# Performance work log

Hardware: AMD Instinct MI355X
Metric: run time of the kernel (lower is better)

Reference implementation:

```python
import jax, jax.numpy as jnp
import numpy as np

D_MODEL = 4096
D_FF = 14336
T = 8192


def setup_inputs() -> dict:
    key = jax.random.key(0)
    k1, k2, k3, k4, k5 = jax.random.split(key, 5)
    s_in = 1.0 / np.sqrt(D_MODEL)
    s_ff = 1.0 / np.sqrt(D_FF)
    return {
        "hidden_states": jax.random.normal(k1, (T, D_MODEL), dtype=jnp.float32),
        "routing_weights": jax.random.uniform(k2, (T, 1), dtype=jnp.float32),
        "w_gate": jax.random.normal(k3, (D_MODEL, D_FF), dtype=jnp.float32) * s_in,
        "w_up": jax.random.normal(k4, (D_MODEL, D_FF), dtype=jnp.float32) * s_in,
        "w_down": jax.random.normal(k5, (D_FF, D_MODEL), dtype=jnp.float32) * s_ff,
    }


def reference(hidden_states, routing_weights, w_gate, w_up, w_down):
    # SwiGLU expert MLP: down(silu(gate(x)) * up(x)), scaled by routing weight
    gate = jnp.einsum("td,df->tf", hidden_states, w_gate)  # [T, D_FF]
    up = jnp.einsum("td,df->tf", hidden_states, w_up)      # [T, D_FF]
    h = jax.nn.silu(gate) * up                               # fused SwiGLU
    out = jnp.einsum("tf,fd->td", h, w_down)                 # [T, D_MODEL]
    return routing_weights * out
```

## Files before the change

### kernel.cpp

```cpp
#include <hip/hip_runtime.h>
#include <hip/hip_bf16.h>

using bf16 = __hip_bfloat16;
typedef __attribute__((ext_vector_type(8))) short bf16x8;
typedef __attribute__((ext_vector_type(4))) float f32x4;
typedef __attribute__((ext_vector_type(4))) int i32x4;

#define T_DIM 8192
#define DM    4096
#define DFF   14336

#define MFMA(va, vb, vc) __builtin_amdgcn_mfma_f32_16x16x32_bf16(va, vb, vc, 0, 0, 0)

__device__ __forceinline__ void gld_lds16(const bf16* gsrc, bf16* ldst) {
  auto* g = (const __attribute__((address_space(1))) unsigned int*)gsrc;
  auto* l = (__attribute__((address_space(3))) unsigned int*)ldst;
  __builtin_amdgcn_global_load_lds(g, l, 16, 0, 0);
}

__device__ __forceinline__ void stage8k(const bf16* __restrict__ gbase, long lda,
                                        long grow0, long k0, bf16* lds_tile,
                                        int gran0, int tid) {
  const int g = gran0 + tid;
  const int row = g >> 3, c16 = g & 7;
  const bf16* src = gbase + (grow0 + row) * lda + k0 + ((long)(c16 ^ (row & 7)) << 3);
  bf16* dst = lds_tile + ((size_t)(gran0 + (tid & ~63)) << 3);
  gld_lds16(src, dst);
}

#define LDA8(PB, H, M, KK) (*(const bf16x8*)(aP##KK + (PB) + (H) * 16384 + (M) * 4096))
#define LDB8(PB, N, KK)    (*(const bf16x8*)(bP##KK + (PB) + (N) * 8192))

#define PHASE_MFMA_BEGIN()                            \
  __builtin_amdgcn_s_barrier();                       \
  asm volatile("s_waitcnt lgkmcnt(0)" ::: "memory");  \
  __builtin_amdgcn_sched_barrier(0);                  \
  __builtin_amdgcn_s_setprio(1)

#define PHASE_MFMA_END()                              \
  __builtin_amdgcn_s_setprio(0);                      \
  __builtin_amdgcn_sched_barrier(0);                  \
  __builtin_amdgcn_s_barrier()

__global__ void cast_pad_kernel(const float* __restrict__ in,
                                bf16* __restrict__ out, long xlda, int n8) {
  int idx = blockIdx.x * blockDim.x + threadIdx.x;
  int stride = gridDim.x * blockDim.x;
  for (int i = idx; i < n8; i += stride) {
    const int row = i >> 9;
    const int c8 = i & 511;
    const float4 v0 = reinterpret_cast<const float4*>(in)[(long)i * 2];
    const float4 v1 = reinterpret_cast<const float4*>(in)[(long)i * 2 + 1];
    bf16 t[8] = {__float2bfloat16(v0.x), __float2bfloat16(v0.y),
                 __float2bfloat16(v0.z), __float2bfloat16(v0.w),
                 __float2bfloat16(v1.x), __float2bfloat16(v1.y),
                 __float2bfloat16(v1.z), __float2bfloat16(v1.w)};
    *reinterpret_cast<bf16x8*>(&out[(long)row * xlda + (long)c8 * 8]) =
        *reinterpret_cast<bf16x8*>(t);
  }
}

__global__ void transpose_cast_kernel(const float* __restrict__ in,
                                      bf16* __restrict__ out, int R, int C,
                                      long out_lda) {
  __shared__ float tile[32][33];
  const int c0 = blockIdx.x * 32, r0 = blockIdx.y * 32;
  const int tx = threadIdx.x, ty = threadIdx.y;
#pragma unroll
  for (int j = 0; j < 4; ++j)
    tile[ty + j * 8][tx] = in[(long)(r0 + ty + j * 8) * C + (c0 + tx)];
  __syncthreads();
#pragma unroll
  for (int j = 0; j < 4; ++j)
    out[(long)(c0 + ty + j * 8) * out_lda + (r0 + tx)] =
        __float2bfloat16(tile[tx][ty + j * 8]);
}

__global__ __launch_bounds__(512, 2) void gemm_gateup_kernel(
    const bf16* __restrict__ X, const bf16* __restrict__ Gt,
    const bf16* __restrict__ Ut, bf16* __restrict__ H,
    long ldx, long ldw, long ldh) {
  __shared__ __align__(16) bf16 smem[4 * 256 * 64];

  const int tid = threadIdx.x;
  const int lane = tid & 63, wid = tid >> 6;
  const int wm = wid >> 2, wn = wid & 3;
  const int fr = lane & 15, fg = lane >> 4;

  const int id = blockIdx.x;
  const int fsub = id & 7, bm = id >> 3;
  const long row0 = (long)bm * 256;
  const int NK = DM / 64;

  bf16* const sAb = smem;
  bf16* const sBb = smem + 32768;

  const int inner0 = ((fg ^ (fr & 7)) << 4);
  const int inner1 = (((4 | fg) ^ (fr & 7)) << 4);
  const char* aP0 = (const char*)sAb + ((wm * 16 + fr) << 7) + inner0;
  const char* aP1 = (const char*)sAb + ((wm * 16 + fr) << 7) + inner1;
  const char* bP0 = (const char*)sBb + ((wn * 16 + fr) << 7) + inner0;
  const char* bP1 = (const char*)sBb + ((wn * 16 + fr) << 7) + inner1;

  const int r6 = tid >> 3;
  const long sc = (long)((tid & 7) ^ (r6 & 7)) << 3;
  const int tu = tid & ~63;
  const bf16* pS0 = X + (row0 + 128 + r6) * ldx + 64 + sc;
  const bf16* pS1 = X + (row0 + 192 + r6) * ldx + 64 + sc;
  const bf16* pS2 = X + (row0 +       r6) * ldx + 128 + sc;
  const bf16* pS3 = X + (row0 +  64 + r6) * ldx + 128 + sc;
  long fcol0 = (long)fsub * 128;
  const bf16* pS4 = Gt + (fcol0 +      r6) * ldw + 128 + sc;
  const bf16* pS5 = Gt + (fcol0 + 64 + r6) * ldw + 128 + sc;
  const bf16* pS6 = Ut + (fcol0 +      r6) * ldw + 128 + sc;
  const bf16* pS7 = Ut + (fcol0 + 64 + r6) * ldw + 128 + sc;

  for (int fb = 0; fb < 14; ++fb) {
    __builtin_amdgcn_s_barrier();

    f32x4 acc[8][4];
    const f32x4 z = {0.f, 0.f, 0.f, 0.f};
#pragma unroll
    for (int m = 0; m < 8; ++m)
#pragma unroll
      for (int n = 0; n < 4; ++n) acc[m][n] = z;

    stage8k(X, ldx, row0, 0, sAb, 0, tid);
    stage8k(X, ldx, row0, 0, sAb, 512, tid);
    stage8k(X, ldx, row0, 0, sAb, 1024, tid);
    stage8k(X, ldx, row0, 0, sAb, 1536, tid);
    stage8k(Gt, ldw, fcol0, 0, sBb, 0, tid);
    stage8k(Gt, ldw, fcol0, 0, sBb, 512, tid);
    stage8k(Ut, ldw, fcol0 - 128, 0, sBb, 1024, tid);
    stage8k(Ut, ldw, fcol0 - 128, 0, sBb, 1536, tid);
    stage8k(X, ldx, row0, 64, sAb + 16384, 0, tid);
    stage8k(X, ldx, row0, 64, sAb + 16384, 512, tid);
    stage8k(Gt, ldw, fcol0, 64, sBb + 16384, 0, tid);
    stage8k(Gt, ldw, fcol0, 64, sBb + 16384, 512, tid);
    stage8k(Ut, ldw, fcol0 - 128, 64, sBb + 16384, 1024, tid);
    stage8k(Ut, ldw, fcol0 - 128, 64, sBb + 16384, 1536, tid);
    asm volatile("s_waitcnt vmcnt(6)" ::: "memory");
    __builtin_amdgcn_s_barrier();

    bf16x8 a[4][2], b[4][2];
    int k1 = 64, k2 = 128;

#pragma unroll 2
    for (int t = 0; t < NK; ++t) {
      const int par = t & 1;
      const int pb = par << 15;
      bf16* aCur = sAb + par * 16384;
      bf16* bCur = sBb + par * 16384;
      bf16* aNxt = sAb + (par ^ 1) * 16384;

#pragma unroll
      for (int m = 0; m < 4; ++m) { a[m][0] = LDA8(pb, 0, m, 0); a[m][1] = LDA8(pb, 0, m, 1); }
#pragma unroll
      for (int n = 0; n < 2; ++n) { b[n][0] = LDB8(pb, n, 0); b[n][1] = LDB8(pb, n, 1); }
      gld_lds16(pS0, aNxt + ((1024 + tu) << 3));
      gld_lds16(pS1, aNxt + ((1536 + tu) << 3));
      PHASE_MFMA_BEGIN();
#pragma unroll
      for (int m = 0; m < 4; ++m)
#pragma unroll
        for (int n = 0; n < 2; ++n)
#pragma unroll
          for (int kk = 0; kk < 2; ++kk)
            acc[m][n] = MFMA(a[m][kk], b[n][kk], acc[m][n]);
      PHASE_MFMA_END();

#pragma unroll
      for (int n = 2; n < 4; ++n) { b[n][0] = LDB8(pb, n, 0); b[n][1] = LDB8(pb, n, 1); }
      gld_lds16(pS2, aCur + ((0 + tu) << 3));
      gld_lds16(pS3, aCur + ((512 + tu) << 3));
      PHASE_MFMA_BEGIN();
#pragma unroll
      for (int m = 0; m < 4; ++m)
#pragma unroll
        for (int n = 2; n < 4; ++n)
#pragma unroll
          for (int kk = 0; kk < 2; ++kk)
            acc[m][n] = MFMA(a[m][kk], b[n][kk], acc[m][n]);
      PHASE_MFMA_END();

#pragma unroll
      for (int m = 0; m < 4; ++m) { a[m][0] = LDA8(pb, 1, m, 0); a[m][1] = LDA8(pb, 1, m, 1); }
      gld_lds16(pS4, bCur + ((0 + tu) << 3));
      gld_lds16(pS5, bCur + ((512 + tu) << 3));
      PHASE_MFMA_BEGIN();
#pragma unroll
      for (int m = 0; m < 4; ++m)
#pragma unroll
        for (int n = 2; n < 4; ++n)
#pragma unroll
          for (int kk = 0; kk < 2; ++kk)
            acc[4 + m][n] = MFMA(a[m][kk], b[n][kk], acc[4 + m][n]);
      PHASE_MFMA_END();

      gld_lds16(pS6, bCur + ((1024 + tu) << 3));
      gld_lds16(pS7, bCur + ((1536 + tu) << 3));
      asm volatile("s_waitcnt vmcnt(6)" ::: "memory");
      PHASE_MFMA_BEGIN();
#pragma unroll
      for (int m = 0; m < 4; ++m)
#pragma unroll
        for (int n = 0; n < 2; ++n)
#pragma unroll
          for (int kk = 0; kk < 2; ++kk)
            acc[4 + m][n] = MFMA(a[m][kk], b[n][kk], acc[4 + m][n]);
      PHASE_MFMA_END();

      pS0 += 64; pS1 += 64;
      k1 += 64;
      if (k1 == DM) { k1 = 0; pS0 -= DM; pS1 -= DM; }
      pS2 += 64; pS3 += 64; pS4 += 64; pS5 += 64; pS6 += 64; pS7 += 64;
      k2 += 64;
      if (k2 == DM) { k2 = 0; pS2 -= DM; pS3 -= DM; pS4 -= DM; pS5 -= DM; pS6 -= DM; pS7 -= DM; }
    }

    asm volatile("s_waitcnt vmcnt(0)" ::: "memory");
    __builtin_amdgcn_s_barrier();

    const int ROWP = 136;
#pragma unroll
    for (int m = 0; m < 8; ++m) {
      const int lr = m * 32 + wm * 16 + fg * 4;
#pragma unroll
      for (int n = 0; n < 2; ++n) {
        const int lc = n * 64 + wn * 16 + fr;
#pragma unroll
        for (int i = 0; i < 4; ++i) {
          float gv = acc[m][n][i];
          float uv = acc[m][n + 2][i];
          float hv = (gv / (1.0f + __expf(-gv))) * uv;
          smem[(lr + i) * ROWP + lc] = __float2bfloat16(hv);
        }
      }
    }
    asm volatile("s_waitcnt lgkmcnt(0)" ::: "memory");
    __builtin_amdgcn_s_barrier();

    {
      const int c16 = tid & 15;
      const int rb = tid >> 4;
#pragma unroll
      for (int it = 0; it < 8; ++it) {
        const int row = rb + it * 32;
        i32x4 v = *(const i32x4*)&smem[row * ROWP + c16 * 8];
        i32x4* dst = (i32x4*)(H + (row0 + row) * ldh + fcol0 + c16 * 8);
        __builtin_nontemporal_store(v, dst);
      }
    }

    fcol0 += 8 * 128;
    pS4 += 8 * 128 * ldw; pS5 += 8 * 128 * ldw;
    pS6 += 8 * 128 * ldw; pS7 += 8 * 128 * ldw;
  }
}

__global__ __launch_bounds__(512, 2) void gemm_down_kernel(
    const bf16* __restrict__ A, const bf16* __restrict__ Bt,
    const float* __restrict__ routing, float* __restrict__ out,
    long ldh, long lddt) {
  __shared__ __align__(16) bf16 sA[2][256 * 64];
  __shared__ __align__(16) bf16 sB[2][256 * 64];

  const int tid = threadIdx.x;
  const int lane = tid & 63, wid = tid >> 6;
  const int wm = wid >> 2, wn = wid & 3;
  const int fr = lane & 15, fg = lane >> 4;

  const int id = blockIdx.x;
  const int xcd = id & 7, j = id >> 3;
  const int bm = j >> 1, bnl = j & 1;
  const long row0 = (long)bm * 256;
  const long col0 = (long)(xcd * 2 + bnl) * 256;
  const int NK = DFF / 64;

  const int inner0 = ((fg ^ (fr & 7)) << 4);
  const int inner1 = (((4 | fg) ^ (fr & 7)) << 4);
  const char* aP0 = (const char*)&sA[0][0] + ((wm * 16 + fr) << 7) + inner0;
  const char* aP1 = (const char*)&sA[0][0] + ((wm * 16 + fr) << 7) + inner1;
  const char* bP0 = (const char*)&sB[0][0] + ((wn * 16 + fr) << 7) + inner0;
  const char* bP1 = (const char*)&sB[0][0] + ((wn * 16 + fr) << 7) + inner1;

  const int r6 = tid >> 3;
  const long sc = (long)((tid & 7) ^ (r6 & 7)) << 3;
  const int tu = tid & ~63;
  const bf16* pS0 = A  + (row0 + 128 + r6) * ldh  + 64 + sc;
  const bf16* pS1 = A  + (row0 + 192 + r6) * ldh  + 64 + sc;
  const bf16* pS2 = A  + (row0 +       r6) * ldh  + 128 + sc;
  const bf16* pS3 = A  + (row0 +  64 + r6) * ldh  + 128 + sc;
  const bf16* pS4 = Bt + (col0 +       r6) * lddt + 128 + sc;
  const bf16* pS5 = Bt + (col0 +  64 + r6) * lddt + 128 + sc;
  const bf16* pS6 = Bt + (col0 + 128 + r6) * lddt + 128 + sc;
  const bf16* pS7 = Bt + (col0 + 192 + r6) * lddt + 128 + sc;

  f32x4 acc[8][4];
  const f32x4 z = {0.f, 0.f, 0.f, 0.f};
#pragma unroll
  for (int m = 0; m < 8; ++m)
#pragma unroll
    for (int n = 0; n < 4; ++n) acc[m][n] = z;

  stage8k(A, ldh, row0, 0, (bf16*)sA[0], 0, tid);
  stage8k(A, ldh, row0, 0, (bf16*)sA[0], 512, tid);
  stage8k(A, ldh, row0, 0, (bf16*)sA[0], 1024, tid);
  stage8k(A, ldh, row0, 0, (bf16*)sA[0], 1536, tid);
  stage8k(Bt, lddt, col0, 0, (bf16*)sB[0], 0, tid);
  stage8k(Bt, lddt, col0, 0, (bf16*)sB[0], 512, tid);
  stage8k(Bt, lddt, col0, 0, (bf16*)sB[0], 1024, tid);
  stage8k(Bt, lddt, col0, 0, (bf16*)sB[0], 1536, tid);
  stage8k(A, ldh, row0, 64, (bf16*)sA[1], 0, tid);
  stage8k(A, ldh, row0, 64, (bf16*)sA[1], 512, tid);
  stage8k(Bt, lddt, col0, 64, (bf16*)sB[1], 0, tid);
  stage8k(Bt, lddt, col0, 64, (bf16*)sB[1], 512, tid);
  stage8k(Bt, lddt, col0, 64, (bf16*)sB[1], 1024, tid);
  stage8k(Bt, lddt, col0, 64, (bf16*)sB[1], 1536, tid);
  asm volatile("s_waitcnt vmcnt(6)" ::: "memory");
  __builtin_amdgcn_s_barrier();

  bf16x8 a[4][2], b[4][2];
  int k1 = 64, k2 = 128;

#pragma unroll 2
  for (int t = 0; t < NK; ++t) {
    const int par = t & 1;
    const int pb = par << 15;
    bf16* aCur = (bf16*)sA[par];
    bf16* bCur = (bf16*)sB[par];
    bf16* aNxt = (bf16*)sA[par ^ 1];

#pragma unroll
    for (int m = 0; m < 4; ++m) { a[m][0] = LDA8(pb, 0, m, 0); a[m][1] = LDA8(pb, 0, m, 1); }
#pragma unroll
    for (int n = 0; n < 2; ++n) { b[n][0] = LDB8(pb, n, 0); b[n][1] = LDB8(pb, n, 1); }
    gld_lds16(pS0, aNxt + ((1024 + tu) << 3));
    gld_lds16(pS1, aNxt + ((1536 + tu) << 3));
    PHASE_MFMA_BEGIN();
#pragma unroll
    for (int m = 0; m < 4; ++m)
#pragma unroll
      for (int n = 0; n < 2; ++n)
#pragma unroll
        for (int kk = 0; kk < 2; ++kk)
          acc[m][n] = MFMA(a[m][kk], b[n][kk], acc[m][n]);
    PHASE_MFMA_END();

#pragma unroll
    for (int n = 2; n < 4; ++n) { b[n][0] = LDB8(pb, n, 0); b[n][1] = LDB8(pb, n, 1); }
    gld_lds16(pS2, aCur + ((0 + tu) << 3));
    gld_lds16(pS3, aCur + ((512 + tu) << 3));
    PHASE_MFMA_BEGIN();
#pragma unroll
    for (int m = 0; m < 4; ++m)
#pragma unroll
      for (int n = 2; n < 4; ++n)
#pragma unroll
        for (int kk = 0; kk < 2; ++kk)
          acc[m][n] = MFMA(a[m][kk], b[n][kk], acc[m][n]);
    PHASE_MFMA_END();

#pragma unroll
    for (int m = 0; m < 4; ++m) { a[m][0] = LDA8(pb, 1, m, 0); a[m][1] = LDA8(pb, 1, m, 1); }
    gld_lds16(pS4, bCur + ((0 + tu) << 3));
    gld_lds16(pS5, bCur + ((512 + tu) << 3));
    PHASE_MFMA_BEGIN();
#pragma unroll
    for (int m = 0; m < 4; ++m)
#pragma unroll
      for (int n = 2; n < 4; ++n)
#pragma unroll
        for (int kk = 0; kk < 2; ++kk)
          acc[4 + m][n] = MFMA(a[m][kk], b[n][kk], acc[4 + m][n]);
    PHASE_MFMA_END();

    gld_lds16(pS6, bCur + ((1024 + tu) << 3));
    gld_lds16(pS7, bCur + ((1536 + tu) << 3));
    asm volatile("s_waitcnt vmcnt(6)" ::: "memory");
    PHASE_MFMA_BEGIN();
#pragma unroll
    for (int m = 0; m < 4; ++m)
#pragma unroll
      for (int n = 0; n < 2; ++n)
#pragma unroll
        for (int kk = 0; kk < 2; ++kk)
          acc[4 + m][n] = MFMA(a[m][kk], b[n][kk], acc[4 + m][n]);
    PHASE_MFMA_END();

    pS0 += 64; pS1 += 64;
    k1 += 64;
    if (k1 == DFF) { k1 = 0; pS0 -= DFF; pS1 -= DFF; }
    pS2 += 64; pS3 += 64; pS4 += 64; pS5 += 64; pS6 += 64; pS7 += 64;
    k2 += 64;
    if (k2 == DFF) { k2 = 0; pS2 -= DFF; pS3 -= DFF; pS4 -= DFF; pS5 -= DFF; pS6 -= DFF; pS7 -= DFF; }
  }

#pragma unroll
  for (int m = 0; m < 8; ++m) {
    const long r0w = row0 + m * 32 + wm * 16 + fg * 4;
#pragma unroll
    for (int i = 0; i < 4; ++i) {
      const long r = r0w + i;
      const float rv = routing[r];
#pragma unroll
      for (int n = 0; n < 4; ++n)
        out[r * DM + (col0 + n * 64 + wn * 16 + fr)] = rv * acc[m][n][i];
    }
  }
}

extern "C" void kernel_launch(void* const* d_in, const int* in_sizes, int n_in,
                              void* d_out, int out_size, void* d_ws, size_t ws_size,
                              hipStream_t stream) {
  const float* X  = (const float*)d_in[0];
  const float* rw = (const float*)d_in[1];
  const float* Wg = (const float*)d_in[2];
  const float* Wu = (const float*)d_in[3];
  const float* Wd = (const float*)d_in[4];
  float* out = (float*)d_out;

  long XL = DM + 64, WL = DM + 64, DL = DFF + 64, HL = DFF + 64;
  {
    size_t need = 2ull * ((size_t)T_DIM * XL + 2ull * (size_t)DFF * WL +
                          (size_t)DM * DL + (size_t)T_DIM * HL);
    if (ws_size < need) { XL = DM; WL = DM; DL = DFF; HL = DFF; }
  }

  char* ws = (char*)d_ws;
  size_t off = 0;
  bf16* Xb = (bf16*)(ws + off); off += (size_t)T_DIM * XL * 2;
  bf16* GT = (bf16*)(ws + off); off += (size_t)DFF * WL * 2;
  bf16* UT = (bf16*)(ws + off); off += (size_t)DFF * WL * 2;
  bf16* DT = (bf16*)(ws + off); off += (size_t)DM * DL * 2;
  bf16* Hb = (bf16*)(ws + off); off += (size_t)T_DIM * HL * 2;

  cast_pad_kernel<<<2048, 256, 0, stream>>>(X, Xb, XL, T_DIM * DM / 8);
  dim3 tpb(32, 8);
  transpose_cast_kernel<<<dim3(DFF / 32, DM / 32), tpb, 0, stream>>>(Wg, GT, DM, DFF, WL);
  transpose_cast_kernel<<<dim3(DFF / 32, DM / 32), tpb, 0, stream>>>(Wu, UT, DM, DFF, WL);
  transpose_cast_kernel<<<dim3(DM / 32, DFF / 32), tpb, 0, stream>>>(Wd, DT, DFF, DM, DL);

  gemm_gateup_kernel<<<256, 512, 0, stream>>>(Xb, GT, UT, Hb, XL, WL, HL);
  gemm_down_kernel<<<(T_DIM / 256) * (DM / 256), 512, 0, stream>>>(
      Hb, DT, rw, out, HL, DL);
}
```

Before: 2.662 ms.

## Fuse gate/up tile loop into one continuous K pipeline with in-loop epilogue

Flattens the 14 output-column tiles and their K loops into a single 896-iteration loop, so the prefetch pipeline keeps running across tile boundaries. The pointers jump straight to the next weight column block, and the SwiGLU epilogue runs every 64 iterations through a separate LDS staging buffer in four 64-row chunks. This removes the per-tile pipeline drain, re-prime and vmcnt(0) stall. In exchange it uses more LDS, adds barriers inside the epilogue while loads are in flight, and the in-loop branch may raise register pressure.

```diff
diff --git a/kernel.cpp b/kernel.cpp
--- a/kernel.cpp
+++ b/kernel.cpp
@@ -80,7 +80,7 @@
     const bf16* __restrict__ X, const bf16* __restrict__ Gt,
     const bf16* __restrict__ Ut, bf16* __restrict__ H,
     long ldx, long ldw, long ldh) {
-  __shared__ __align__(16) bf16 smem[4 * 256 * 64];
+  __shared__ __align__(16) bf16 smem[4 * 256 * 64 + 64 * 136];
 
   const int tid = threadIdx.x;
   const int lane = tid & 63, wid = tid >> 6;
@@ -90,10 +90,10 @@
   const int id = blockIdx.x;
   const int fsub = id & 7, bm = id >> 3;
   const long row0 = (long)bm * 256;
-  const int NK = DM / 64;
 
   bf16* const sAb = smem;
   bf16* const sBb = smem + 32768;
+  bf16* const sEp = smem + 65536;
 
   const int inner0 = ((fg ^ (fr & 7)) << 4);
   const int inner1 = (((4 | fg) ^ (fr & 7)) << 4);
@@ -114,147 +114,148 @@
   const bf16* pS5 = Gt + (fcol0 + 64 + r6) * ldw + 128 + sc;
   const bf16* pS6 = Ut + (fcol0 +      r6) * ldw + 128 + sc;
   const bf16* pS7 = Ut + (fcol0 + 64 + r6) * ldw + 128 + sc;
-
-  for (int fb = 0; fb < 14; ++fb) {
-    __builtin_amdgcn_s_barrier();
-
-    f32x4 acc[8][4];
-    const f32x4 z = {0.f, 0.f, 0.f, 0.f};
-#pragma unroll
-    for (int m = 0; m < 8; ++m)
-#pragma unroll
-      for (int n = 0; n < 4; ++n) acc[m][n] = z;
-
-    stage8k(X, ldx, row0, 0, sAb, 0, tid);
-    stage8k(X, ldx, row0, 0, sAb, 512, tid);
-    stage8k(X, ldx, row0, 0, sAb, 1024, tid);
-    stage8k(X, ldx, row0, 0, sAb, 1536, tid);
-    stage8k(Gt, ldw, fcol0, 0, sBb, 0, tid);
-    stage8k(Gt, ldw, fcol0, 0, sBb, 512, tid);
-    stage8k(Ut, ldw, fcol0 - 128, 0, sBb, 1024, tid);
-    stage8k(Ut, ldw, fcol0 - 128, 0, sBb, 1536, tid);
-    stage8k(X, ldx, row0, 64, sAb + 16384, 0, tid);
-    stage8k(X, ldx, row0, 64, sAb + 16384, 512, tid);
-    stage8k(Gt, ldw, fcol0, 64, sBb + 16384, 0, tid);
-    stage8k(Gt, ldw, fcol0, 64, sBb + 16384, 512, tid);
-    stage8k(Ut, ldw, fcol0 - 128, 64, sBb + 16384, 1024, tid);
-    stage8k(Ut, ldw, fcol0 - 128, 64, sBb + 16384, 1536, tid);
+  const long BJMP = 1024 * ldw - DM;
+  long fcolH = fcol0;
+
+  f32x4 acc[8][4];
+  const f32x4 z = {0.f, 0.f, 0.f, 0.f};
+#pragma unroll
+  for (int m = 0; m < 8; ++m)
+#pragma unroll
+    for (int n = 0; n < 4; ++n) acc[m][n] = z;
+
+  stage8k(X, ldx, row0, 0, sAb, 0, tid);
+  stage8k(X, ldx, row0, 0, sAb, 512, tid);
+  stage8k(X, ldx, row0, 0, sAb, 1024, tid);
+  stage8k(X, ldx, row0, 0, sAb, 1536, tid);
+  stage8k(Gt, ldw, fcol0, 0, sBb, 0, tid);
+  stage8k(Gt, ldw, fcol0, 0, sBb, 512, tid);
+  stage8k(Ut, ldw, fcol0 - 128, 0, sBb, 1024, tid);
+  stage8k(Ut, ldw, fcol0 - 128, 0, sBb, 1536, tid);
+  stage8k(X, ldx, row0, 64, sAb + 16384, 0, tid);
+  stage8k(X, ldx, row0, 64, sAb + 16384, 512, tid);
+  stage8k(Gt, ldw, fcol0, 64, sBb + 16384, 0, tid);
+  stage8k(Gt, ldw, fcol0, 64, sBb + 16384, 512, tid);
+  stage8k(Ut, ldw, fcol0 - 128, 64, sBb + 16384, 1024, tid);
+  stage8k(Ut, ldw, fcol0 - 128, 64, sBb + 16384, 1536, tid);
+  asm volatile("s_waitcnt vmcnt(6)" ::: "memory");
+  __builtin_amdgcn_s_barrier();
+
+  bf16x8 a[4][2], b[4][2];
+  int k1 = 64, k2 = 128;
+
+#pragma unroll 2
+  for (int g = 0; g < 896; ++g) {
+    const int par = g & 1;
+    const int pb = par << 15;
+    bf16* aCur = sAb + par * 16384;
+    bf16* bCur = sBb + par * 16384;
+    bf16* aNxt = sAb + (par ^ 1) * 16384;
+
+#pragma unroll
+    for (int m = 0; m < 4; ++m) { a[m][0] = LDA8(pb, 0, m, 0); a[m][1] = LDA8(pb, 0, m, 1); }
+#pragma unroll
+    for (int n = 0; n < 2; ++n) { b[n][0] = LDB8(pb, n, 0); b[n][1] = LDB8(pb, n, 1); }
+    gld_lds16(pS0, aNxt + ((1024 + tu) << 3));
+    gld_lds16(pS1, aNxt + ((1536 + tu) << 3));
+    PHASE_MFMA_BEGIN();
+#pragma unroll
+    for (int m = 0; m < 4; ++m)
+#pragma unroll
+      for (int n = 0; n < 2; ++n)
+#pragma unroll
+        for (int kk = 0; kk < 2; ++kk)
+          acc[m][n] = MFMA(a[m][kk], b[n][kk], acc[m][n]);
+    PHASE_MFMA_END();
+
+#pragma unroll
+    for (int n = 2; n < 4; ++n) { b[n][0] = LDB8(pb, n, 0); b[n][1] = LDB8(pb, n, 1); }
+    gld_lds16(pS2, aCur + ((0 + tu) << 3));
+    gld_lds16(pS3, aCur + ((512 + tu) << 3));
+    PHASE_MFMA_BEGIN();
+#pragma unroll
+    for (int m = 0; m < 4; ++m)
+#pragma unroll
+      for (int n = 2; n < 4; ++n)
+#pragma unroll
+        for (int kk = 0; kk < 2; ++kk)
+          acc[m][n] = MFMA(a[m][kk], b[n][kk], acc[m][n]);
+    PHASE_MFMA_END();
+
+#pragma unroll
+    for (int m = 0; m < 4; ++m) { a[m][0] = LDA8(pb, 1, m, 0); a[m][1] = LDA8(pb, 1, m, 1); }
+    gld_lds16(pS4, bCur + ((0 + tu) << 3));
+    gld_lds16(pS5, bCur + ((512 + tu) << 3));
+    PHASE_MFMA_BEGIN();
+#pragma unroll
+    for (int m = 0; m < 4; ++m)
+#pragma unroll
+      for (int n = 2; n < 4; ++n)
+#pragma unroll
+        for (int kk = 0; kk < 2; ++kk)
+          acc[4 + m][n] = MFMA(a[m][kk], b[n][kk], acc[4 + m][n]);
+    PHASE_MFMA_END();
+
+    gld_lds16(pS6, bCur + ((1024 + tu) << 3));
+    gld_lds16(pS7, bCur + ((1536 + tu) << 3));
     asm volatile("s_waitcnt vmcnt(6)" ::: "memory");
-    __builtin_amdgcn_s_barrier();
-
-    bf16x8 a[4][2], b[4][2];
-    int k1 = 64, k2 = 128;
-
-#pragma unroll 2
-    for (int t = 0; t < NK; ++t) {
-      const int par = t & 1;
-      const int pb = par << 15;
-      bf16* aCur = sAb + par * 16384;
-      bf16* bCur = sBb + par * 16384;
-      bf16* aNxt = sAb + (par ^ 1) * 16384;
-
-#pragma unroll
-      for (int m = 0; m < 4; ++m) { a[m][0] = LDA8(pb, 0, m, 0); a[m][1] = LDA8(pb, 0, m, 1); }
-#pragma unroll
-      for (int n = 0; n < 2; ++n) { b[n][0] = LDB8(pb, n, 0); b[n][1] = LDB8(pb, n, 1); }
-      gld_lds16(pS0, aNxt + ((1024 + tu) << 3));
-      gld_lds16(pS1, aNxt + ((1536 + tu) << 3));
-      PHASE_MFMA_BEGIN();
-#pragma unroll
-      for (int m = 0; m < 4; ++m)
-#pragma unroll
-        for (int n = 0; n < 2; ++n)
-#pragma unroll
-          for (int kk = 0; kk < 2; ++kk)
-            acc[m][n] = MFMA(a[m][kk], b[n][kk], acc[m][n]);
-      PHASE_MFMA_END();
-
-#pragma unroll
-      for (int n = 2; n < 4; ++n) { b[n][0] = LDB8(pb, n, 0); b[n][1] = LDB8(pb, n, 1); }
-      gld_lds16(pS2, aCur + ((0 + tu) << 3));
-      gld_lds16(pS3, aCur + ((512 + tu) << 3));
-      PHASE_MFMA_BEGIN();
-#pragma unroll
-      for (int m = 0; m < 4; ++m)
-#pragma unroll
-        for (int n = 2; n < 4; ++n)
-#pragma unroll
-          for (int kk = 0; kk < 2; ++kk)
-            acc[m][n] = MFMA(a[m][kk], b[n][kk], acc[m][n]);
-      PHASE_MFMA_END();
-
-#pragma unroll
-      for (int m = 0; m < 4; ++m) { a[m][0] = LDA8(pb, 1, m, 0); a[m][1] = LDA8(pb, 1, m, 1); }
-      gld_lds16(pS4, bCur + ((0 + tu) << 3));
-      gld_lds16(pS5, bCur + ((512 + tu) << 3));
-      PHASE_MFMA_BEGIN();
-#pragma unroll
-      for (int m = 0; m < 4; ++m)
-#pragma unroll
-        for (int n = 2; n < 4; ++n)
-#pragma unroll
-          for (int kk = 0; kk < 2; ++kk)
-            acc[4 + m][n] = MFMA(a[m][kk], b[n][kk], acc[4 + m][n]);
-      PHASE_MFMA_END();
-
-      gld_lds16(pS6, bCur + ((1024 + tu) << 3));
-      gld_lds16(pS7, bCur + ((1536 + tu) << 3));
-      asm volatile("s_waitcnt vmcnt(6)" ::: "memory");
-      PHASE_MFMA_BEGIN();
-#pragma unroll
-      for (int m = 0; m < 4; ++m)
-#pragma unroll
-        for (int n = 0; n < 2; ++n)
-#pragma unroll
-          for (int kk = 0; kk < 2; ++kk)
-            acc[4 + m][n] = MFMA(a[m][kk], b[n][kk], acc[4 + m][n]);
-      PHASE_MFMA_END();
-
-      pS0 += 64; pS1 += 64;
-      k1 += 64;
-      if (k1 == DM) { k1 = 0; pS0 -= DM; pS1 -= DM; }
-      pS2 += 64; pS3 += 64; pS4 += 64; pS5 += 64; pS6 += 64; pS7 += 64;
-      k2 += 64;
-      if (k2 == DM) { k2 = 0; pS2 -= DM; pS3 -= DM; pS4 -= DM; pS5 -= DM; pS6 -= DM; pS7 -= DM; }
+    PHASE_MFMA_BEGIN();
+#pragma unroll
+    for (int m = 0; m < 4; ++m)
+#pragma unroll
+      for (int n = 0; n < 2; ++n)
+#pragma unroll
+        for (int kk = 0; kk < 2; ++kk)
+          acc[4 + m][n] = MFMA(a[m][kk], b[n][kk], acc[4 + m][n]);
+    PHASE_MFMA_END();
+
+    pS0 += 64; pS1 += 64;
+    k1 += 64;
+    if (k1 == DM) { k1 = 0; pS0 -= DM; pS1 -= DM; }
+    pS2 += 64; pS3 += 64; pS4 += 64; pS5 += 64; pS6 += 64; pS7 += 64;
+    k2 += 64;
+    if (k2 == DM) {
+      k2 = 0; pS2 -= DM; pS3 -= DM;
+      pS4 += BJMP; pS5 += BJMP; pS6 += BJMP; pS7 += BJMP;
     }
 
-    asm volatile("s_waitcnt vmcnt(0)" ::: "memory");
-    __builtin_amdgcn_s_barrier();
-
-    const int ROWP = 136;
-#pragma unroll
-    for (int m = 0; m < 8; ++m) {
-      const int lr = m * 32 + wm * 16 + fg * 4;
-#pragma unroll
-      for (int n = 0; n < 2; ++n) {
-        const int lc = n * 64 + wn * 16 + fr;
-#pragma unroll
-        for (int i = 0; i < 4; ++i) {
-          float gv = acc[m][n][i];
-          float uv = acc[m][n + 2][i];
-          float hv = (gv / (1.0f + __expf(-gv))) * uv;
-          smem[(lr + i) * ROWP + lc] = __float2bfloat16(hv);
+    if ((g & 63) == 63) {
+#pragma unroll
+      for (int q = 0; q < 4; ++q) {
+        __builtin_amdgcn_s_barrier();
+#pragma unroll
+        for (int mm = 0; mm < 2; ++mm) {
+          const int m = 2 * q + mm;
+          const int lr = mm * 32 + wm * 16 + fg * 4;
+#pragma unroll
+          for (int n = 0; n < 2; ++n) {
+            const int lc = n * 64 + wn * 16 + fr;
+#pragma unroll
+            for (int i = 0; i < 4; ++i) {
+              float gv = acc[m][n][i];
+              float uv = acc[m][n + 2][i];
+              float hv = (gv / (1.0f + __expf(-gv))) * uv;
+              sEp[(lr + i) * 136 + lc] = __float2bfloat16(hv);
+              acc[m][n][i] = 0.f;
+              acc[m][n + 2][i] = 0.f;
+            }
+          }
+        }
+        asm volatile("s_waitcnt lgkmcnt(0)" ::: "memory");
+        __builtin_amdgcn_s_barrier();
+        {
+          const int c16 = tid & 15, rb = tid >> 4;
+#pragma unroll
+          for (int it = 0; it < 2; ++it) {
+            const int lr = rb + it * 32;
+            i32x4 v = *(const i32x4*)&sEp[lr * 136 + c16 * 8];
+            __builtin_nontemporal_store(
+                v, (i32x4*)(H + (row0 + q * 64 + lr) * ldh + fcolH + c16 * 8));
+          }
         }
       }
+      fcolH += 1024;
     }
-    asm volatile("s_waitcnt lgkmcnt(0)" ::: "memory");
-    __builtin_amdgcn_s_barrier();
-
-    {
-      const int c16 = tid & 15;
-      const int rb = tid >> 4;
-#pragma unroll
-      for (int it = 0; it < 8; ++it) {
-        const int row = rb + it * 32;
-        i32x4 v = *(const i32x4*)&smem[row * ROWP + c16 * 8];
-        i32x4* dst = (i32x4*)(H + (row0 + row) * ldh + fcol0 + c16 * 8);
-        __builtin_nontemporal_store(v, dst);
-      }
-    }
-
-    fcol0 += 8 * 128;
-    pS4 += 8 * 128 * ldw; pS5 += 8 * 128 * ldw;
-    pS6 += 8 * 128 * ldw; pS7 += 8 * 128 * ldw;
   }
 }
 
```

Result: faster. 2.592 ms (-2.6%).
